# Performance work log

Hardware: AMD Instinct MI355X
Metric: run time of the kernel (lower is better)

## Reference

```python
import math
import jax, jax.numpy as jnp
import numpy as np

B, NH, L0 = 16, 128, 16384
KS, STRIDE = 4, 2
INIT_GATE_BIAS = 1.0


def _num_steps(L, ks, stride):
    # number of reduce steps until any N <= L reaches N <= 1 (matches torch N recurrence)
    d, n = 0, L
    while True:
        n = (max(n - ks, 0) + stride - 1) // stride + 1
        d += 1
        if n <= 1:
            return d


def setup_inputs() -> dict:
    key = jax.random.key(0)
    k1, k2, k3, k4 = jax.random.split(key, 4)
    h = jax.random.normal(k1, (B, NH, L0), dtype=jnp.float32)
    N = jax.random.randint(k2, (B,), 1, L0 + 1, dtype=jnp.int32)
    cin = NH + 1  # depth_variant adds one channel
    bound = 1.0 / math.sqrt(cin * KS)
    W = jax.random.uniform(k3, (3 * NH, cin, KS), minval=-bound, maxval=bound, dtype=jnp.float32)
    b = jax.random.uniform(k4, (3 * NH,), minval=-bound, maxval=bound, dtype=jnp.float32)
    b = b.at[2 * NH:].set(INIT_GATE_BIAS)
    return {"h": h, "N": N, "W": W, "b": b}


def _step(h, N, depth, W, b):
    Bb, _, Lc = h.shape
    # depth channel (depth_variant=True), then mask invalid positions (mask applied after concat, as in torch)
    d = jnp.full((Bb, 1, Lc), math.log1p(depth), dtype=h.dtype)
    hh = jnp.concatenate([h, d], axis=1)
    mask = (jnp.arange(Lc) < N[:, None]).astype(hh.dtype)  # [B, Lc]
    hh = hh * mask[:, None, :]
    # right-pad so conv covers all valid positions
    if Lc < KS:
        pad_r = KS - Lc
    elif (Lc - KS) % STRIDE != 0:
        pad_r = STRIDE - (Lc - KS) % STRIDE
    else:
        pad_r = 0
    if pad_r:
        hh = jnp.pad(hh, ((0, 0), (0, 0), (0, pad_r)))
    lrg = jax.lax.conv_general_dilated(
        hh, W, window_strides=(STRIDE,), padding='VALID',
        dimension_numbers=('NCH', 'OIH', 'NCH')) + b[None, :, None]
    l = lrg[:, :NH]
    r = jnp.tanh(lrg[:, NH:2 * NH])
    g = jax.nn.sigmoid(lrg[:, 2 * NH:])
    h_new = l * g + r * (1.0 - g)
    m = jnp.maximum(N - KS, 0)
    N_new = (m + STRIDE - 1) // STRIDE + 1  # ceil(clamp(N-ks,0)/stride)+1
    return h_new, N_new


def reference(h, N, W, b):
    # Fixed-depth unroll: instead of compacting the batch (dynamic shapes), run
    # every sample for all D steps and record its row at the step it finishes.
    # Torch output order = samples sorted stably by finish depth (boolean-index
    # compaction preserves original relative order), reproduced via stable argsort.
    D = _num_steps(h.shape[2], KS, STRIDE)
    Bb = h.shape[0]
    out_h = jnp.zeros((Bb, NH), dtype=h.dtype)
    finish = jnp.full((Bb,), D, dtype=jnp.int32)
    done = jnp.zeros((Bb,), dtype=bool)
    for depth in range(D):
        h, N = _step(h, N, depth, W, b)
        newly = (~done) & (N <= 1)
        out_h = jnp.where(newly[:, None], h[:, :, 0], out_h)
        finish = jnp.where(newly, depth, finish)
        done = done | newly
    order = jnp.argsort(finish)  # stable by default in jax
    return out_h[order]
```

## Files before the change

kernel.cpp:

```cpp
#include <hip/hip_runtime.h>
#include <math.h>

typedef _Float16 f16_t;
typedef _Float16 f16x8 __attribute__((ext_vector_type(8)));
typedef _Float16 f16x4 __attribute__((ext_vector_type(4)));
typedef float    f32x4 __attribute__((ext_vector_type(4)));

#define NHC 128
#define NBATCH 16
#define JT 64
#define THREADS 512
#define LDSROWPITCH 272
#define LDSREGION (66*LDSROWPITCH)

__device__ __host__ __forceinline__ int nstep_f(int n){ int m = n - 4; m = m < 0 ? 0 : m; return ((m + 1) >> 1) + 1; }

__global__ void prep_kernel(const float* __restrict__ W, const float* __restrict__ bin,
                            f16_t* __restrict__ Wt, float* __restrict__ Pp, float* __restrict__ biasf)
{
    int c = blockIdx.x;
    int i = threadIdx.x;
    #pragma unroll
    for (int k = 0; k < 4; k++)
        Wt[((size_t)k*384 + c)*128 + i] = (f16_t)W[((size_t)c*129 + i)*4 + k];
    if (i == 0) {
        float s = 0.f;
        Pp[c*5 + 0] = 0.f;
        #pragma unroll
        for (int k = 0; k < 4; k++) { s += W[((size_t)c*129 + 128)*4 + k]; Pp[c*5 + k + 1] = s; }
        biasf[c] = bin[c];
    }
}

__global__ void transpose_kernel(const float* __restrict__ h, const int* __restrict__ N0,
                                 f16_t* __restrict__ X0, int outCols)
{
    __shared__ float tile[32][65];
    const int b = blockIdx.z, c0 = blockIdx.y*32, p0 = blockIdx.x*64;
    const int tid = threadIdx.x;
    const int n0 = N0[b];
    const int L0c = 16384;
    {
        int c = tid >> 3, pc = (tid & 7) * 8;
        const float* src = h + ((size_t)b*NHC + c0 + c)*L0c + p0 + pc;
        float4 v0 = *(const float4*)(src);
        float4 v1 = *(const float4*)(src + 4);
        *(float4*)(&tile[c][pc])     = v0;
        *(float4*)(&tile[c][pc + 4]) = v1;
    }
    __syncthreads();
    {
        int p = tid >> 2, cc = (tid & 3) * 8;
        bool dead = (p0 + p >= n0);
        f16x8 vv;
        #pragma unroll
        for (int e = 0; e < 8; e++) vv[e] = dead ? (f16_t)0.f : (f16_t)tile[cc + e][p];
        *(f16x8*)(X0 + ((size_t)b*outCols + p0 + p)*NHC + c0 + cc) = vv;
    }
}

template<int CTM>
__device__ __forceinline__ void gemm_tap(f32x4 (&acc)[3][4], const f16_t* __restrict__ Wt,
                                         const char* ldsIn, int arow, int n16, int q)
{
    #pragma unroll 1
    for (int k = 0; k < 4; k++) {
        const f16_t* ab = Wt + ((size_t)k*384 + arow)*128 + q*8;
        f16x8 a0[4], a1[4], a2[4];
        #pragma unroll
        for (int kc = 0; kc < 4; kc++) {
            a0[kc] = *(const f16x8*)(ab + kc*32);
            a1[kc] = *(const f16x8*)(ab + 16384 + kc*32);
            a2[kc] = *(const f16x8*)(ab + 32768 + kc*32);
        }
        const char* bb0 = ldsIn + (k&1)*LDSREGION + ((k>>1) + n16)*LDSROWPITCH + q*16;
        #pragma unroll
        for (int kc = 0; kc < 4; kc++) {
            #pragma unroll
            for (int ct = 0; ct < CTM; ct++) {
                f16x8 bb = *(const f16x8*)(bb0 + ct*(16*LDSROWPITCH) + kc*64);
                acc[0][ct] = __builtin_amdgcn_mfma_f32_16x16x32_f16(a0[kc], bb, acc[0][ct], 0, 0, 0);
                acc[1][ct] = __builtin_amdgcn_mfma_f32_16x16x32_f16(a1[kc], bb, acc[1][ct], 0, 0, 0);
                acc[2][ct] = __builtin_amdgcn_mfma_f32_16x16x32_f16(a2[kc], bb, acc[2][ct], 0, 0, 0);
            }
        }
    }
}

__device__ __forceinline__ void load_biasp(float (&biasr)[3][4], float (&pfull)[3][4],
                                           const float* __restrict__ biasf,
                                           const float* __restrict__ Pp, int cw)
{
    #pragma unroll
    for (int s = 0; s < 3; s++)
        #pragma unroll
        for (int r = 0; r < 4; r++) {
            int row = s*128 + cw + r;
            biasr[s][r] = biasf[row];
            pfull[s][r] = Pp[row*5 + 4];
        }
}

template<int CTE, bool TO_LDS>
__device__ __forceinline__ void epilogue_store(
    const f32x4 (&acc)[3][4], char* ldsOut, f16_t* goutB,
    const float (&biasr)[3][4], const float (&pfull)[3][4],
    const float* __restrict__ Pp, float* __restrict__ outrow,
    int j0, int Nt, int Nt1, float dval, bool record, int n16, int cw)
{
    #pragma unroll
    for (int ct = 0; ct < CTE; ct++) {
        int j = j0 + ct*16 + n16;
        int cnt = Nt - 2*j; cnt = cnt < 0 ? 0 : (cnt > 4 ? 4 : cnt);
        bool zero = (j >= Nt1);
        float hv[4];
        #pragma unroll
        for (int r = 0; r < 4; r++) {
            float d0, d1, d2;
            if (cnt == 4)      { d0 = pfull[0][r]; d1 = pfull[1][r]; d2 = pfull[2][r]; }
            else if (cnt == 0) { d0 = 0.f; d1 = 0.f; d2 = 0.f; }
            else { int rw = cw + r; d0 = Pp[rw*5 + cnt]; d1 = Pp[(128+rw)*5 + cnt]; d2 = Pp[(256+rw)*5 + cnt]; }
            float lv = acc[0][ct][r] + biasr[0][r] + dval*d0;
            float rp = acc[1][ct][r] + biasr[1][r] + dval*d1;
            float gp = acc[2][ct][r] + biasr[2][r] + dval*d2;
            float e2 = __expf(2.f*rp);
            float rv = 1.f - 2.f/(e2 + 1.f);
            float gv = 1.f/(1.f + __expf(-gp));
            float hh = lv*gv + rv*(1.f - gv);
            hv[r] = zero ? 0.f : hh;
        }
        f16x4 hb;
        #pragma unroll
        for (int r = 0; r < 4; r++) hb[r] = (f16_t)hv[r];
        if constexpr (TO_LDS) {
            *(f16x4*)(ldsOut + (j&1)*LDSREGION + (j>>1)*LDSROWPITCH + cw*2) = hb;
        } else {
            *(f16x4*)(goutB + (ct*16 + n16)*NHC + cw) = hb;
        }
        if (record && ct == 0 && n16 == 0) {
            #pragma unroll
            for (int r = 0; r < 4; r++) outrow[cw + r] = hv[r];
        }
    }
}

__global__ __launch_bounds__(THREADS) void conv_kernel(
    const f16_t* __restrict__ Xin, f16_t* __restrict__ Xout,
    const f16_t* __restrict__ Wt, const float* __restrict__ Pp,
    const float* __restrict__ biasf, const int* __restrict__ N0,
    float* __restrict__ outbuf,
    int t, int inCols, int outCols, float dval)
{
    __shared__ alignas(16) char ldsX[2*LDSREGION];
    const int b  = blockIdx.y;
    const int j0 = blockIdx.x * JT;
    const int tid = threadIdx.x;
    int Nt = N0[b];
    for (int s = 0; s < t; s++) Nt = nstep_f(Nt);
    const int Nt1 = nstep_f(Nt);

    f16_t* XoutB = Xout + ((size_t)b*outCols + j0)*NHC;
    if (j0 >= Nt1) {
        float4 z = {0.f,0.f,0.f,0.f};
        float4* p = (float4*)XoutB;
        #pragma unroll
        for (int i = 0; i < 2; i++) p[i*THREADS + tid] = z;
        return;
    }

    const int w    = tid >> 6;
    const int lane = tid & 63;
    const int n16  = lane & 15;
    const int q    = lane >> 4;
    const int arow = w*16 + n16;
    const int cw   = w*16 + q*4;

    const char* XinB = (const char*)(Xin + ((size_t)b*inCols + 2*(size_t)j0)*NHC);
    const int maxrow = inCols - 2*j0;
    for (int it = 0; it < 5; ++it) {
        int idx = it*THREADS + tid;
        if (idx < 130*16) {
            int row = idx >> 4, cb = (idx & 15) * 16;
            float4 v = {0.f,0.f,0.f,0.f};
            if (row < maxrow) v = *(const float4*)(XinB + row*256 + cb);
            *(float4*)(ldsX + (row&1)*LDSREGION + (row>>1)*LDSROWPITCH + cb) = v;
        }
    }
    __syncthreads();

    f32x4 acc[3][4] = {};
    int ctm = (Nt1 - j0 + 15) >> 4; if (ctm > 4) ctm = 4;
    switch (ctm) {
    case 1:  gemm_tap<1>(acc, Wt, ldsX, arow, n16, q); break;
    case 2:  gemm_tap<2>(acc, Wt, ldsX, arow, n16, q); break;
    case 3:  gemm_tap<3>(acc, Wt, ldsX, arow, n16, q); break;
    default: gemm_tap<4>(acc, Wt, ldsX, arow, n16, q); break;
    }

    float biasr[3][4], pfull[3][4];
    load_biasp(biasr, pfull, biasf, Pp, cw);

    bool newly = (Nt1 == 1) && (t == 0 || Nt > 1);
    epilogue_store<4, false>(acc, nullptr, XoutB, biasr, pfull, Pp, outbuf + b*NHC,
                             j0, Nt, Nt1, dval, newly && (j0 == 0), n16, cw);
}

template<int CTM>
__device__ __forceinline__ void tail_iter(
    char* ldsX, const f16_t* __restrict__ Wt,
    const float (&biasr)[3][4], const float (&pfull)[3][4],
    const float* __restrict__ Pp, float* __restrict__ outrow,
    int n16, int q, int arow, int cw, int Nt, int Nt1, float dval, bool newly)
{
    f32x4 acc[3][4] = {};
    gemm_tap<CTM>(acc, Wt, ldsX, arow, n16, q);
    __syncthreads();
    epilogue_store<CTM, true>(acc, ldsX, nullptr, biasr, pfull, Pp, outrow,
                              0, Nt, Nt1, dval, newly, n16, cw);
}

__global__ __launch_bounds__(THREADS) void tail_kernel(
    const f16_t* __restrict__ Xin, const f16_t* __restrict__ Wt,
    const float* __restrict__ Pp, const float* __restrict__ biasf,
    const int* __restrict__ N0, float* __restrict__ outbuf, int inCols)
{
    __shared__ alignas(16) char ldsX[2*LDSREGION];
    const int b = blockIdx.x;
    const int tid = threadIdx.x;
    int Nt = N0[b];
    for (int s = 0; s < 7; s++) Nt = nstep_f(Nt);
    if (Nt <= 1) return;

    const int w    = tid >> 6;
    const int lane = tid & 63;
    const int n16  = lane & 15;
    const int q    = lane >> 4;
    const int arow = w*16 + n16;
    const int cw   = w*16 + q*4;
    float* outrow  = outbuf + b*NHC;

    const char* XinB = (const char*)(Xin + (size_t)b*inCols*NHC);
    for (int it = 0; it < 5; ++it) {
        int idx = it*THREADS + tid;
        if (idx < 130*16) {
            int row = idx >> 4, cb = (idx & 15) * 16;
            float4 v = {0.f,0.f,0.f,0.f};
            if (row < inCols) v = *(const float4*)(XinB + row*256 + cb);
            *(float4*)(ldsX + (row&1)*LDSREGION + (row>>1)*LDSROWPITCH + cb) = v;
        }
    }

    float biasr[3][4], pfull[3][4];
    load_biasp(biasr, pfull, biasf, Pp, cw);
    __syncthreads();

    for (int t = 7; t < 13; ++t) {
        int Nt1 = nstep_f(Nt);
        bool newly = (Nt1 == 1);
        float dval = log1pf((float)t);
        int ctmax = (Nt1 >> 4) + 1; if (ctmax > 4) ctmax = 4;
        switch (ctmax) {
        case 1:  tail_iter<1>(ldsX, Wt, biasr, pfull, Pp, outrow, n16, q, arow, cw, Nt, Nt1, dval, newly); break;
        case 2:  tail_iter<2>(ldsX, Wt, biasr, pfull, Pp, outrow, n16, q, arow, cw, Nt, Nt1, dval, newly); break;
        case 3:  tail_iter<3>(ldsX, Wt, biasr, pfull, Pp, outrow, n16, q, arow, cw, Nt, Nt1, dval, newly); break;
        default: tail_iter<4>(ldsX, Wt, biasr, pfull, Pp, outrow, n16, q, arow, cw, Nt, Nt1, dval, newly); break;
        }
        if (newly) return;
        Nt = Nt1;
        __syncthreads();
    }
}

__global__ void finalize_kernel(const float* __restrict__ outbuf,
                                const int* __restrict__ N0, float* __restrict__ dout)
{
    __shared__ int fin[16];
    __shared__ int rnk[16];
    int tid = threadIdx.x;
    if (tid < 16) {
        int n = N0[tid]; int f = 12;
        for (int t = 0; t < 13; t++) { n = nstep_f(n); if (n == 1) { f = t; break; } }
        fin[tid] = f;
    }
    __syncthreads();
    if (tid < 16) {
        int r = 0;
        for (int b2 = 0; b2 < 16; b2++)
            if (fin[b2] < fin[tid] || (fin[b2] == fin[tid] && b2 < tid)) r++;
        rnk[tid] = r;
    }
    __syncthreads();
    for (int e = tid; e < NBATCH*NHC; e += 256) {
        int b = e >> 7, c = e & 127;
        dout[rnk[b]*NHC + c] = outbuf[e];
    }
}

extern "C" void kernel_launch(void* const* d_in, const int* in_sizes, int n_in,
                              void* d_out, int out_size, void* d_ws, size_t ws_size,
                              hipStream_t stream)
{
    const float* h    = (const float*)d_in[0];
    const int*   N0   = (const int*)d_in[1];
    const float* W    = (const float*)d_in[2];
    const float* bvec = (const float*)d_in[3];
    float* dout = (float*)d_out;

    int Ls[14], Ms[14];
    Ls[0] = 16384;
    for (int t = 0; t < 13; t++) Ls[t+1] = nstep_f(Ls[t]);
    for (int t = 0; t < 14; t++) Ms[t] = ((Ls[t] + 63) / 64) * 64;

    char* ws = (char*)d_ws;
    size_t off = 0;
    auto alloc = [&](size_t bytes){ size_t o = off; off += (bytes + 255) & ~(size_t)255; return o; };
    size_t oXA   = alloc((size_t)NBATCH * Ms[0] * NHC * 2);
    size_t oXB   = alloc((size_t)NBATCH * Ms[1] * NHC * 2);
    size_t oWt   = alloc((size_t)4*384*128*2);
    size_t oPp   = alloc((size_t)384*5*4);
    size_t oBias = alloc((size_t)384*4);
    size_t oOut  = alloc((size_t)NBATCH*NHC*4);
    f16_t* XA    = (f16_t*)(ws + oXA);
    f16_t* XB    = (f16_t*)(ws + oXB);
    f16_t* Wt    = (f16_t*)(ws + oWt);
    float* Pp    = (float*)(ws + oPp);
    float* biasf = (float*)(ws + oBias);
    float* outb  = (float*)(ws + oOut);

    hipLaunchKernelGGL(prep_kernel, dim3(384), dim3(128), 0, stream, W, bvec, Wt, Pp, biasf);
    hipLaunchKernelGGL(transpose_kernel, dim3(Ms[0]/64, 4, NBATCH), dim3(256), 0, stream, h, N0, XA, Ms[0]);

    f16_t* cur = XA; f16_t* nxt = XB;
    for (int t = 0; t < 7; t++) {
        hipLaunchKernelGGL(conv_kernel, dim3(Ms[t+1]/64, NBATCH), dim3(THREADS), 0, stream,
                           cur, nxt, Wt, Pp, biasf, N0, outb, t, Ms[t], Ms[t+1], log1pf((float)t));
        f16_t* tmp = cur; cur = nxt; nxt = tmp;
    }
    hipLaunchKernelGGL(tail_kernel, dim3(NBATCH), dim3(THREADS), 0, stream,
                       cur, Wt, Pp, biasf, N0, outb, Ms[7]);
    hipLaunchKernelGGL(finalize_kernel, dim3(1), dim3(256), 0, stream, outb, N0, dout);
}
```

Measured before the change: 498.6 us.

## Fuse input transpose into first conv step and extend tail kernel by one level

Removes the separate transpose kernel. The first conv launch now reads fp32 h directly from global memory, converts it to fp16 and writes the transposed tile into LDS, so the full-size fp16 copy of the input is no longer written and re-read. The tail kernel now starts one step earlier (t=6) with a larger LDS region and up to 8 column tiles, split into two gemm passes, which removes one conv launch. The trade-offs are a strided, less coalesced float2 global read pattern in the first step, and more LDS and serial work in the single-block-per-batch tail kernel.

```diff
diff --git a/kernel.cpp b/kernel.cpp
--- a/kernel.cpp
+++ b/kernel.cpp
@@ -10,8 +10,10 @@
 #define NBATCH 16
 #define JT 64
 #define THREADS 512
+#define L0LEN 16384
 #define LDSROWPITCH 272
 #define LDSREGION (66*LDSROWPITCH)
+#define TREGION (130*LDSROWPITCH)
 
 __device__ __host__ __forceinline__ int nstep_f(int n){ int m = n - 4; m = m < 0 ? 0 : m; return ((m + 1) >> 1) + 1; }
 
@@ -32,36 +34,9 @@
     }
 }
 
-__global__ void transpose_kernel(const float* __restrict__ h, const int* __restrict__ N0,
-                                 f16_t* __restrict__ X0, int outCols)
-{
-    __shared__ float tile[32][65];
-    const int b = blockIdx.z, c0 = blockIdx.y*32, p0 = blockIdx.x*64;
-    const int tid = threadIdx.x;
-    const int n0 = N0[b];
-    const int L0c = 16384;
-    {
-        int c = tid >> 3, pc = (tid & 7) * 8;
-        const float* src = h + ((size_t)b*NHC + c0 + c)*L0c + p0 + pc;
-        float4 v0 = *(const float4*)(src);
-        float4 v1 = *(const float4*)(src + 4);
-        *(float4*)(&tile[c][pc])     = v0;
-        *(float4*)(&tile[c][pc + 4]) = v1;
-    }
-    __syncthreads();
-    {
-        int p = tid >> 2, cc = (tid & 3) * 8;
-        bool dead = (p0 + p >= n0);
-        f16x8 vv;
-        #pragma unroll
-        for (int e = 0; e < 8; e++) vv[e] = dead ? (f16_t)0.f : (f16_t)tile[cc + e][p];
-        *(f16x8*)(X0 + ((size_t)b*outCols + p0 + p)*NHC + c0 + cc) = vv;
-    }
-}
-
-template<int CTM>
+template<int REG, int CTM>
 __device__ __forceinline__ void gemm_tap(f32x4 (&acc)[3][4], const f16_t* __restrict__ Wt,
-                                         const char* ldsIn, int arow, int n16, int q)
+                                         const char* ldsIn, int arow, int n16, int q, int jt)
 {
     #pragma unroll 1
     for (int k = 0; k < 4; k++) {
@@ -73,7 +48,7 @@
             a1[kc] = *(const f16x8*)(ab + 16384 + kc*32);
             a2[kc] = *(const f16x8*)(ab + 32768 + kc*32);
         }
-        const char* bb0 = ldsIn + (k&1)*LDSREGION + ((k>>1) + n16)*LDSROWPITCH + q*16;
+        const char* bb0 = ldsIn + (k&1)*REG + ((k>>1) + n16 + jt*16)*LDSROWPITCH + q*16;
         #pragma unroll
         for (int kc = 0; kc < 4; kc++) {
             #pragma unroll
@@ -101,7 +76,7 @@
         }
 }
 
-template<int CTE, bool TO_LDS>
+template<int REG, int CTE, bool TO_LDS>
 __device__ __forceinline__ void epilogue_store(
     const f32x4 (&acc)[3][4], char* ldsOut, f16_t* goutB,
     const float (&biasr)[3][4], const float (&pfull)[3][4],
@@ -133,7 +108,7 @@
         #pragma unroll
         for (int r = 0; r < 4; r++) hb[r] = (f16_t)hv[r];
         if constexpr (TO_LDS) {
-            *(f16x4*)(ldsOut + (j&1)*LDSREGION + (j>>1)*LDSROWPITCH + cw*2) = hb;
+            *(f16x4*)(ldsOut + (j&1)*REG + (j>>1)*LDSROWPITCH + cw*2) = hb;
         } else {
             *(f16x4*)(goutB + (ct*16 + n16)*NHC + cw) = hb;
         }
@@ -145,7 +120,7 @@
 }
 
 __global__ __launch_bounds__(THREADS) void conv_kernel(
-    const f16_t* __restrict__ Xin, f16_t* __restrict__ Xout,
+    const float* __restrict__ h, const f16_t* __restrict__ Xin, f16_t* __restrict__ Xout,
     const f16_t* __restrict__ Wt, const float* __restrict__ Pp,
     const float* __restrict__ biasf, const int* __restrict__ N0,
     float* __restrict__ outbuf,
@@ -168,6 +143,47 @@
         return;
     }
 
+    if (t == 0) {
+        const float* hB = h + (size_t)b*NHC*L0LEN;
+        const int P0 = 2*j0;
+        const int jpr = tid & 63;
+        const int s8  = tid >> 6;
+        #pragma unroll
+        for (int cg = 0; cg < 16; cg++) {
+            int c = cg*8 + s8;
+            int p = P0 + jpr*2;
+            float2 v = {0.f, 0.f};
+            if (p + 1 < Nt)      v = *(const float2*)(hB + (size_t)c*L0LEN + p);
+            else if (p < Nt)     v.x = hB[(size_t)c*L0LEN + p];
+            char* wb = ldsX + jpr*LDSROWPITCH + c*2;
+            *(f16_t*)(wb)             = (f16_t)v.x;
+            *(f16_t*)(wb + LDSREGION) = (f16_t)v.y;
+        }
+        if (tid < 128) {
+            int c = tid;
+            int p = P0 + 128;
+            float2 v = {0.f, 0.f};
+            if (p + 1 < Nt)      v = *(const float2*)(hB + (size_t)c*L0LEN + p);
+            else if (p < Nt)     v.x = hB[(size_t)c*L0LEN + p];
+            char* wb = ldsX + 64*LDSROWPITCH + c*2;
+            *(f16_t*)(wb)             = (f16_t)v.x;
+            *(f16_t*)(wb + LDSREGION) = (f16_t)v.y;
+        }
+    } else {
+        const char* XinB = (const char*)(Xin + ((size_t)b*inCols + 2*(size_t)j0)*NHC);
+        const int maxrow = inCols - 2*j0;
+        for (int it = 0; it < 5; ++it) {
+            int idx = it*THREADS + tid;
+            if (idx < 130*16) {
+                int row = idx >> 4, cb = (idx & 15) * 16;
+                float4 v = {0.f,0.f,0.f,0.f};
+                if (row < maxrow) v = *(const float4*)(XinB + row*256 + cb);
+                *(float4*)(ldsX + (row&1)*LDSREGION + (row>>1)*LDSROWPITCH + cb) = v;
+            }
+        }
+    }
+    __syncthreads();
+
     const int w    = tid >> 6;
     const int lane = tid & 63;
     const int n16  = lane & 15;
@@ -175,48 +191,35 @@
     const int arow = w*16 + n16;
     const int cw   = w*16 + q*4;
 
-    const char* XinB = (const char*)(Xin + ((size_t)b*inCols + 2*(size_t)j0)*NHC);
-    const int maxrow = inCols - 2*j0;
-    for (int it = 0; it < 5; ++it) {
-        int idx = it*THREADS + tid;
-        if (idx < 130*16) {
-            int row = idx >> 4, cb = (idx & 15) * 16;
-            float4 v = {0.f,0.f,0.f,0.f};
-            if (row < maxrow) v = *(const float4*)(XinB + row*256 + cb);
-            *(float4*)(ldsX + (row&1)*LDSREGION + (row>>1)*LDSROWPITCH + cb) = v;
-        }
-    }
-    __syncthreads();
-
     f32x4 acc[3][4] = {};
     int ctm = (Nt1 - j0 + 15) >> 4; if (ctm > 4) ctm = 4;
     switch (ctm) {
-    case 1:  gemm_tap<1>(acc, Wt, ldsX, arow, n16, q); break;
-    case 2:  gemm_tap<2>(acc, Wt, ldsX, arow, n16, q); break;
-    case 3:  gemm_tap<3>(acc, Wt, ldsX, arow, n16, q); break;
-    default: gemm_tap<4>(acc, Wt, ldsX, arow, n16, q); break;
+    case 1:  gemm_tap<LDSREGION,1>(acc, Wt, ldsX, arow, n16, q, 0); break;
+    case 2:  gemm_tap<LDSREGION,2>(acc, Wt, ldsX, arow, n16, q, 0); break;
+    case 3:  gemm_tap<LDSREGION,3>(acc, Wt, ldsX, arow, n16, q, 0); break;
+    default: gemm_tap<LDSREGION,4>(acc, Wt, ldsX, arow, n16, q, 0); break;
     }
 
     float biasr[3][4], pfull[3][4];
     load_biasp(biasr, pfull, biasf, Pp, cw);
 
     bool newly = (Nt1 == 1) && (t == 0 || Nt > 1);
-    epilogue_store<4, false>(acc, nullptr, XoutB, biasr, pfull, Pp, outbuf + b*NHC,
-                             j0, Nt, Nt1, dval, newly && (j0 == 0), n16, cw);
-}
-
-template<int CTM>
+    epilogue_store<LDSREGION,4,false>(acc, nullptr, XoutB, biasr, pfull, Pp, outbuf + b*NHC,
+                                      j0, Nt, Nt1, dval, newly && (j0 == 0), n16, cw);
+}
+
+template<int REG, int CTM>
 __device__ __forceinline__ void tail_iter(
     char* ldsX, const f16_t* __restrict__ Wt,
     const float (&biasr)[3][4], const float (&pfull)[3][4],
     const float* __restrict__ Pp, float* __restrict__ outrow,
-    int n16, int q, int arow, int cw, int Nt, int Nt1, float dval, bool newly)
+    int n16, int q, int arow, int cw, int jt, int Nt, int Nt1, float dval, bool newly)
 {
     f32x4 acc[3][4] = {};
-    gemm_tap<CTM>(acc, Wt, ldsX, arow, n16, q);
-    __syncthreads();
-    epilogue_store<CTM, true>(acc, ldsX, nullptr, biasr, pfull, Pp, outrow,
-                              0, Nt, Nt1, dval, newly, n16, cw);
+    gemm_tap<REG,CTM>(acc, Wt, ldsX, arow, n16, q, jt);
+    __syncthreads();
+    epilogue_store<REG,CTM,true>(acc, ldsX, nullptr, biasr, pfull, Pp, outrow,
+                                 jt*16, Nt, Nt1, dval, newly, n16, cw);
 }
 
 __global__ __launch_bounds__(THREADS) void tail_kernel(
@@ -224,11 +227,11 @@
     const float* __restrict__ Pp, const float* __restrict__ biasf,
     const int* __restrict__ N0, float* __restrict__ outbuf, int inCols)
 {
-    __shared__ alignas(16) char ldsX[2*LDSREGION];
+    __shared__ alignas(16) char ldsX[2*TREGION];
     const int b = blockIdx.x;
     const int tid = threadIdx.x;
     int Nt = N0[b];
-    for (int s = 0; s < 7; s++) Nt = nstep_f(Nt);
+    for (int s = 0; s < 6; s++) Nt = nstep_f(Nt);
     if (Nt <= 1) return;
 
     const int w    = tid >> 6;
@@ -240,30 +243,37 @@
     float* outrow  = outbuf + b*NHC;
 
     const char* XinB = (const char*)(Xin + (size_t)b*inCols*NHC);
-    for (int it = 0; it < 5; ++it) {
+    for (int it = 0; it < 8; ++it) {
         int idx = it*THREADS + tid;
-        if (idx < 130*16) {
-            int row = idx >> 4, cb = (idx & 15) * 16;
-            float4 v = {0.f,0.f,0.f,0.f};
-            if (row < inCols) v = *(const float4*)(XinB + row*256 + cb);
-            *(float4*)(ldsX + (row&1)*LDSREGION + (row>>1)*LDSROWPITCH + cb) = v;
-        }
+        int row = idx >> 4, cb = (idx & 15) * 16;
+        float4 v = {0.f,0.f,0.f,0.f};
+        if (row < inCols) v = *(const float4*)(XinB + row*256 + cb);
+        *(float4*)(ldsX + (row&1)*TREGION + (row>>1)*LDSROWPITCH + cb) = v;
     }
 
     float biasr[3][4], pfull[3][4];
     load_biasp(biasr, pfull, biasf, Pp, cw);
     __syncthreads();
 
-    for (int t = 7; t < 13; ++t) {
+    for (int t = 6; t < 13; ++t) {
         int Nt1 = nstep_f(Nt);
         bool newly = (Nt1 == 1);
         float dval = log1pf((float)t);
-        int ctmax = (Nt1 >> 4) + 1; if (ctmax > 4) ctmax = 4;
-        switch (ctmax) {
-        case 1:  tail_iter<1>(ldsX, Wt, biasr, pfull, Pp, outrow, n16, q, arow, cw, Nt, Nt1, dval, newly); break;
-        case 2:  tail_iter<2>(ldsX, Wt, biasr, pfull, Pp, outrow, n16, q, arow, cw, Nt, Nt1, dval, newly); break;
-        case 3:  tail_iter<3>(ldsX, Wt, biasr, pfull, Pp, outrow, n16, q, arow, cw, Nt, Nt1, dval, newly); break;
-        default: tail_iter<4>(ldsX, Wt, biasr, pfull, Pp, outrow, n16, q, arow, cw, Nt, Nt1, dval, newly); break;
+        int ctmax = (Nt1 >> 4) + 1; if (ctmax > 8) ctmax = 8;
+        int cA = ctmax > 4 ? 4 : ctmax;
+        switch (cA) {
+        case 1:  tail_iter<TREGION,1>(ldsX, Wt, biasr, pfull, Pp, outrow, n16, q, arow, cw, 0, Nt, Nt1, dval, newly); break;
+        case 2:  tail_iter<TREGION,2>(ldsX, Wt, biasr, pfull, Pp, outrow, n16, q, arow, cw, 0, Nt, Nt1, dval, newly); break;
+        case 3:  tail_iter<TREGION,3>(ldsX, Wt, biasr, pfull, Pp, outrow, n16, q, arow, cw, 0, Nt, Nt1, dval, newly); break;
+        default: tail_iter<TREGION,4>(ldsX, Wt, biasr, pfull, Pp, outrow, n16, q, arow, cw, 0, Nt, Nt1, dval, newly); break;
+        }
+        if (ctmax > 4) {
+            switch (ctmax - 4) {
+            case 1:  tail_iter<TREGION,1>(ldsX, Wt, biasr, pfull, Pp, outrow, n16, q, arow, cw, 4, Nt, Nt1, dval, false); break;
+            case 2:  tail_iter<TREGION,2>(ldsX, Wt, biasr, pfull, Pp, outrow, n16, q, arow, cw, 4, Nt, Nt1, dval, false); break;
+            case 3:  tail_iter<TREGION,3>(ldsX, Wt, biasr, pfull, Pp, outrow, n16, q, arow, cw, 4, Nt, Nt1, dval, false); break;
+            default: tail_iter<TREGION,4>(ldsX, Wt, biasr, pfull, Pp, outrow, n16, q, arow, cw, 4, Nt, Nt1, dval, false); break;
+            }
         }
         if (newly) return;
         Nt = Nt1;
@@ -307,15 +317,15 @@
     float* dout = (float*)d_out;
 
     int Ls[14], Ms[14];
-    Ls[0] = 16384;
+    Ls[0] = L0LEN;
     for (int t = 0; t < 13; t++) Ls[t+1] = nstep_f(Ls[t]);
     for (int t = 0; t < 14; t++) Ms[t] = ((Ls[t] + 63) / 64) * 64;
 
     char* ws = (char*)d_ws;
     size_t off = 0;
     auto alloc = [&](size_t bytes){ size_t o = off; off += (bytes + 255) & ~(size_t)255; return o; };
-    size_t oXA   = alloc((size_t)NBATCH * Ms[0] * NHC * 2);
-    size_t oXB   = alloc((size_t)NBATCH * Ms[1] * NHC * 2);
+    size_t oXA   = alloc((size_t)NBATCH * Ms[1] * NHC * 2);
+    size_t oXB   = alloc((size_t)NBATCH * Ms[2] * NHC * 2);
     size_t oWt   = alloc((size_t)4*384*128*2);
     size_t oPp   = alloc((size_t)384*5*4);
     size_t oBias = alloc((size_t)384*4);
@@ -328,15 +338,17 @@
     float* outb  = (float*)(ws + oOut);
 
     hipLaunchKernelGGL(prep_kernel, dim3(384), dim3(128), 0, stream, W, bvec, Wt, Pp, biasf);
-    hipLaunchKernelGGL(transpose_kernel, dim3(Ms[0]/64, 4, NBATCH), dim3(256), 0, stream, h, N0, XA, Ms[0]);
 
     f16_t* cur = XA; f16_t* nxt = XB;
-    for (int t = 0; t < 7; t++) {
+    hipLaunchKernelGGL(conv_kernel, dim3(Ms[1]/64, NBATCH), dim3(THREADS), 0, stream,
+                       h, (const f16_t*)nullptr, XA, Wt, Pp, biasf, N0, outb,
+                       0, Ms[0], Ms[1], log1pf(0.f));
+    for (int t = 1; t < 6; t++) {
         hipLaunchKernelGGL(conv_kernel, dim3(Ms[t+1]/64, NBATCH), dim3(THREADS), 0, stream,
-                           cur, nxt, Wt, Pp, biasf, N0, outb, t, Ms[t], Ms[t+1], log1pf((float)t));
+                           h, cur, nxt, Wt, Pp, biasf, N0, outb, t, Ms[t], Ms[t+1], log1pf((float)t));
         f16_t* tmp = cur; cur = nxt; nxt = tmp;
     }
     hipLaunchKernelGGL(tail_kernel, dim3(NBATCH), dim3(THREADS), 0, stream,
-                       cur, Wt, Pp, biasf, N0, outb, Ms[7]);
+                       cur, Wt, Pp, biasf, N0, outb, Ms[6]);
     hipLaunchKernelGGL(finalize_kernel, dim3(1), dim3(256), 0, stream, outb, N0, dout);
 }
```

Measured after the change: 487.1 us. -2.3%, faster.
